# Kernel optimization log

Hardware: AMD Instinct MI355X
Metric: run time of the kernel (lower is better)

## Reference

```python
import jax, jax.numpy as jnp
import numpy as np
from jax import lax

B, CIN, H, W = 8, 3, 256, 256
CMID = 16          # conv out channels == config.in_channels
DM = 256           # d_model
P = 2              # patch size (hardcoded in Downsample)
DI = 512           # d_inner = expand * d_model
NH, HD, NS, KC = 8, 64, 128, 4   # heads, headdim, d_state, d_conv
CONVDIM = DI + 2 * NS            # 768
PROJ = 2 * DI + 2 * NS + NH      # 1288


def _sincos2d(dim, gs):
    # 2d sin-cos positional embedding, matches get_2d_sincos_pos_embed
    def emb1d(d, pos):
        omega = 1.0 / (10000.0 ** (jnp.arange(d // 2, dtype=jnp.float32) / (d / 2.0)))
        out = pos[:, None] * omega[None, :]
        return jnp.concatenate([jnp.sin(out), jnp.cos(out)], axis=1)
    g = jnp.arange(gs, dtype=jnp.float32)
    grid = jnp.stack(jnp.meshgrid(g, g), 0).reshape(2, -1)  # [2, gs*gs]
    return jnp.concatenate([emb1d(dim // 2, grid[0]), emb1d(dim // 2, grid[1])], 1)


def _mamba2(u, in_proj_w, conv1d_w, conv1d_b, dt_bias, A_log, D, norm_w, out_proj_w):
    b, l, _ = u.shape
    zxbcdt = jnp.einsum('bld,pd->blp', u, in_proj_w)              # [b,l,1288]
    z = zxbcdt[..., :DI]
    xBC = zxbcdt[..., DI:DI + CONVDIM]
    dt = zxbcdt[..., DI + CONVDIM:]                                # [b,l,NH]
    # causal depthwise conv1d over sequence, then SiLU
    xc = lax.conv_general_dilated(xBC.transpose(0, 2, 1), conv1d_w, (1,), [(KC - 1, 0)],
                                  feature_group_count=CONVDIM,
                                  dimension_numbers=('NCH', 'OIH', 'NCH'))
    xBC = jax.nn.silu(xc + conv1d_b[None, :, None]).transpose(0, 2, 1)
    xh = xBC[..., :DI].reshape(b, l, NH, HD)                       # [b,l,h,p]
    Bm = xBC[..., DI:DI + NS]                                      # [b,l,n]
    Cm = xBC[..., DI + NS:]                                        # [b,l,n]
    dt = jax.nn.softplus(dt + dt_bias)                             # [b,l,h]
    dA = jnp.exp(dt * (-jnp.exp(A_log)))                           # [b,l,h]
    dtx = dt[..., None] * xh                                       # [b,l,h,p]

    def step(s, inp):
        dtx_t, B_t, C_t, dA_t = inp
        s = s * dA_t[..., None, None] + dtx_t[..., None] * B_t[:, None, None, :]
        return s, jnp.einsum('bhpn,bn->bhp', s, C_t)

    s0 = jnp.zeros((b, NH, HD, NS), u.dtype)
    _, ys = lax.scan(step, s0, (dtx.transpose(1, 0, 2, 3), Bm.transpose(1, 0, 2),
                                Cm.transpose(1, 0, 2), dA.transpose(1, 0, 2)))
    y = ys.transpose(1, 0, 2, 3) + D[None, None, :, None] * xh     # [b,l,h,p]
    y = y.reshape(b, l, DI) * jax.nn.silu(z)                       # gated
    y = y * lax.rsqrt(jnp.mean(y * y, -1, keepdims=True) + 1e-5) * norm_w
    return jnp.einsum('bld,od->blo', y, out_proj_w)


def setup_inputs() -> dict:
    key = jax.random.key(0)
    ks = jax.random.split(key, 12)
    r = lambda i, s, sc: jax.random.normal(ks[i], s, jnp.float32) * sc
    return {
        'x': jax.random.normal(ks[0], (B, CIN, H, W), jnp.float32),
        'conv_w': r(1, (CMID, CIN, 3, 3), 0.1), 'conv_b': jnp.zeros((CMID,), jnp.float32),
        'bn_gamma': jnp.ones((CMID,), jnp.float32), 'bn_beta': jnp.zeros((CMID,), jnp.float32),
        'patch_w': r(2, (DM, CMID, P, P), 0.1), 'patch_b': jnp.zeros((DM,), jnp.float32),
        'in_proj_w': r(3, (PROJ, DM), 0.02),
        'conv1d_w': r(4, (CONVDIM, 1, KC), 0.1), 'conv1d_b': jnp.zeros((CONVDIM,), jnp.float32),
        'dt_bias': r(5, (NH,), 0.5),
        'A_log': jax.random.uniform(ks[6], (NH,), jnp.float32),
        'D': jnp.ones((NH,), jnp.float32),
        'norm_w': jnp.ones((DI,), jnp.float32),
        'out_proj_w': r(7, (DM, DI), 0.02),
        'final_w': r(8, (P * P * CMID, DM), 0.02), 'final_b': jnp.zeros((P * P * CMID,), jnp.float32),
    }


def reference(x, conv_w, conv_b, bn_gamma, bn_beta, patch_w, patch_b, in_proj_w,
              conv1d_w, conv1d_b, dt_bias, A_log, D, norm_w, out_proj_w, final_w, final_b):
    # Conv2d k=3 s=2 p=1 -> BatchNorm2d (training-mode batch stats) -> GELU
    h = lax.conv_general_dilated(x, conv_w, (2, 2), [(1, 1), (1, 1)],
                                 dimension_numbers=('NCHW', 'OIHW', 'NCHW')) + conv_b[None, :, None, None]
    mu = jnp.mean(h, (0, 2, 3), keepdims=True)
    var = jnp.var(h, (0, 2, 3), keepdims=True)
    h = (h - mu) * lax.rsqrt(var + 1e-5) * bn_gamma[None, :, None, None] + bn_beta[None, :, None, None]
    h = jax.nn.gelu(h, approximate=False)
    # PatchEmbed: conv k=p s=p, flatten to tokens, add frozen sincos pos embed
    t = lax.conv_general_dilated(h, patch_w, (P, P), 'VALID',
                                 dimension_numbers=('NCHW', 'OIHW', 'NCHW')) + patch_b[None, :, None, None]
    b, d, gh, gw = t.shape
    tok = t.reshape(b, d, gh * gw).transpose(0, 2, 1) + _sincos2d(DM, gh)[None]
    # MambaBlock: Mamba2(x) + x  (layers=1; repo loop discards all but last layer)
    y = _mamba2(tok, in_proj_w, conv1d_w, conv1d_b, dt_bias, A_log, D, norm_w, out_proj_w) + tok
    # FinalLayer: linear only (norm_final is unused in its forward)
    o = jnp.einsum('bld,od->blo', y, final_w) + final_b
    # unpatchify
    o = o.reshape(b, gh, gw, P, P, CMID)
    o = jnp.einsum('nhwpqc->nchpwq', o).reshape(b, CMID, gh * P, gw * P)
    return o
```

## Files before the change

kernel.cpp:

```cpp
#include <hip/hip_runtime.h>
#include <math.h>

#define B_  8
#define CIN 3
#define HIN 256
#define WIN 256
#define CMID 16
#define HMID 128
#define WMID 128
#define DM 256
#define L_ 4096
#define DI 512
#define NH 8
#define HD 64
#define NS 128
#define KC 4
#define CONVDIM 768
#define PROJ 1288
#define NPADIN 1408
#define MTOK (B_*L_)
#define QCH 128
#define NCH 32

typedef unsigned short bf16;
typedef __attribute__((ext_vector_type(8))) short bf16x8;
typedef __attribute__((ext_vector_type(4))) float f32x4;

__device__ inline float bf2f(bf16 u) { return __uint_as_float(((unsigned int)u) << 16); }
__device__ inline bf16 f2bf(float f) {
  unsigned int x = __float_as_uint(f);
  return (bf16)((x + 0x7fffu + ((x >> 16) & 1u)) >> 16);
}
__device__ inline unsigned int pack2bf(float a, float b) {
  return (unsigned int)f2bf(a) | ((unsigned int)f2bf(b) << 16);
}

__global__ void k_conv1(const float* __restrict__ x, const float* __restrict__ w,
                        const float* __restrict__ bias, float* __restrict__ out) {
  int idx = blockIdx.x*256 + threadIdx.x;
  if (idx >= B_*CMID*HMID*WMID) return;
  int xo = idx & 127, yo = (idx>>7)&127, co = (idx>>14)&15, b = idx>>18;
  float acc = bias[co];
  const float* xb = x + (size_t)b*CIN*HIN*WIN;
  const float* wc = w + co*CIN*9;
  #pragma unroll
  for (int ci=0; ci<CIN; ci++)
    #pragma unroll
    for (int ky=0; ky<3; ky++) {
      int yi = 2*yo - 1 + ky;
      if (yi < 0 || yi >= HIN) continue;
      #pragma unroll
      for (int kx=0; kx<3; kx++) {
        int xi = 2*xo - 1 + kx;
        if (xi < 0 || xi >= WIN) continue;
        acc += xb[(ci*HIN + yi)*WIN + xi] * wc[(ci*3+ky)*3+kx];
      }
    }
  out[idx] = acc;
}

__global__ __launch_bounds__(256) void k_bnstatsA(const float* __restrict__ h, float2* __restrict__ part) {
  int blk = blockIdx.x;
  const float4* base = (const float4*)(h + ((size_t)(blk>>2))*16384 + (blk&3)*4096);
  int tid = threadIdx.x;
  float s=0.f, s2=0.f;
  #pragma unroll
  for (int i=0;i<4;i++){
    float4 v = base[i*256 + tid];
    s += v.x+v.y+v.z+v.w;
    s2 += v.x*v.x + v.y*v.y + v.z*v.z + v.w*v.w;
  }
  #pragma unroll
  for (int off=1; off<64; off<<=1) { s += __shfl_xor(s, off); s2 += __shfl_xor(s2, off); }
  __shared__ float sb[2][4];
  if ((tid&63)==0){ sb[0][tid>>6]=s; sb[1][tid>>6]=s2; }
  __syncthreads();
  if (tid==0) part[blk] = make_float2(sb[0][0]+sb[0][1]+sb[0][2]+sb[0][3],
                                      sb[1][0]+sb[1][1]+sb[1][2]+sb[1][3]);
}

__global__ void k_bnstatsB(const float2* __restrict__ part, float* __restrict__ stats) {
  int lane = threadIdx.x;
  int c = lane >> 2, j0 = lane & 3;
  float s=0.f, s2=0.f;
  #pragma unroll
  for (int j=j0; j<32; j+=4){
    int b = j >> 2, chunk = j & 3;
    float2 p = part[(b*16+c)*4 + chunk];
    s += p.x; s2 += p.y;
  }
  s += __shfl_xor(s,1); s2 += __shfl_xor(s2,1);
  s += __shfl_xor(s,2); s2 += __shfl_xor(s2,2);
  if (j0==0){
    const float inv = 1.f/131072.f;
    float mean = s*inv;
    float var  = s2*inv - mean*mean;
    stats[c]      = mean;
    stats[16 + c] = rsqrtf(var + 1e-5f);
  }
}

__global__ __launch_bounds__(256) void k_patch(const float* __restrict__ h, const float* __restrict__ pw,
                       const float* __restrict__ pb, const float* __restrict__ stats,
                       const float* __restrict__ gamma, const float* __restrict__ beta,
                       bf16* __restrict__ tok) {
  int grp = blockIdx.x;
  int b = grp >> 9, g8 = grp & 511;
  int g0 = g8 << 3;
  int gy = g0 >> 6, gx0 = g0 & 63;
  __shared__ float sh[8][64];
  int tid = threadIdx.x;
  {
    int tk = tid >> 5, jj = (tid & 31)*2;
    int ci = jj >> 2, p = (jj >> 1) & 1;
    const float* src = &h[((size_t)(b*CMID+ci)*HMID + 2*gy+p)*WMID + 2*(gx0+tk)];
    float2 xv = *(const float2*)src;
    float mean = stats[ci], rstd = stats[16+ci];
    float sc = rstd*gamma[ci], be = beta[ci] - mean*sc;
    float v0 = xv.x*sc + be;
    float v1 = xv.y*sc + be;
    v0 = 0.5f*v0*(1.f + erff(v0*0.70710678118654752f));
    v1 = 0.5f*v1*(1.f + erff(v1*0.70710678118654752f));
    sh[tk][jj] = v0; sh[tk][jj+1] = v1;
  }
  __syncthreads();
  int d = tid;
  float wr[64];
  #pragma unroll
  for (int i4=0;i4<16;i4++) *(float4*)&wr[i4*4] = *(const float4*)&pw[d*64 + i4*4];
  float bias = pb[d];
  int i = d & 63;
  float omega = expf(-(float)i * (9.210340371976184f/64.f));
  #pragma unroll
  for (int tk=0;tk<8;tk++){
    float acc = bias;
    #pragma unroll
    for (int j=0;j<64;j++) acc = fmaf(sh[tk][j], wr[j], acc);
    float gv = (d < 128) ? (float)(gx0+tk) : (float)gy;
    float ph = gv * omega;
    float pos = (d & 64) ? __cosf(ph) : __sinf(ph);
    tok[((size_t)((b<<12) + g0 + tk))*DM + d] = f2bf(acc + pos);
  }
}

__global__ void k_cvtw(const float* __restrict__ src, bf16* __restrict__ dst,
                       int N, int kshift, int total) {
  int idx = blockIdx.x*256 + threadIdx.x;
  if (idx >= total) return;
  int n = idx >> kshift;
  dst[idx] = (n < N) ? f2bf(src[idx]) : (bf16)0;
}

template<int EPI>
__global__ __launch_bounds__(512) void k_mgemm(
    const bf16* __restrict__ A, const bf16* __restrict__ Bw, int K,
    bf16* __restrict__ o_z, bf16* __restrict__ o_x,
    bf16* __restrict__ o_y, const bf16* __restrict__ res,
    const float* __restrict__ dt_bias, const float* __restrict__ A_log,
    float* __restrict__ dtv, float* __restrict__ dAv,
    float* __restrict__ o_f, const float* __restrict__ fbias) {
  __shared__ __align__(16) char smem[49152];
  bf16* sA = (bf16*)smem;
  bf16* sB = (bf16*)(smem + 32768);
  bf16* sT = (bf16*)smem;
  int tid = threadIdx.x;
  int lane = tid & 63, wid = tid >> 6;
  int wr = wid >> 1, wc = wid & 1;
  int m0 = blockIdx.x*256, n0 = blockIdx.y*128;
  int nk = K >> 5;

  f32x4 acc[4][4];
  #pragma unroll
  for (int i=0;i<4;i++)
    #pragma unroll
    for (int j=0;j<4;j++)
      acc[i][j] = (f32x4){0.f,0.f,0.f,0.f};

  auto stage = [&](int buf, int ks){
    int kk = ks << 5;
    #pragma unroll
    for (int i=0;i<2;i++){
      int j = i*512 + tid;
      int row = j >> 2, cc = j & 3;
      int kg = cc ^ (row & 3);
      unsigned ldsoff = (unsigned)(buf*16384 + (i*512 + wid*64) * 16);
      __builtin_amdgcn_global_load_lds(
        (const __attribute__((address_space(1))) void*)(A + (size_t)(m0+row)*K + kk + kg*8),
        (__attribute__((address_space(3))) void*)((char*)sA + ldsoff), 16, 0, 0);
    }
    {
      int row = tid >> 2, cc = tid & 3;
      int kg = cc ^ (row & 3);
      unsigned ldsoff = (unsigned)(buf*8192 + (wid*64) * 16);
      __builtin_amdgcn_global_load_lds(
        (const __attribute__((address_space(1))) void*)(Bw + (size_t)(n0+row)*K + kk + kg*8),
        (__attribute__((address_space(3))) void*)((char*)sB + ldsoff), 16, 0, 0);
    }
  };

  int r = lane & 15, q = lane >> 4;
  int kgo = (q ^ (r & 3)) << 3;

  stage(0, 0);
  for (int ks=0; ks<nk; ++ks){
    int cur = ks & 1;
    __syncthreads();
    if (ks+1 < nk) stage(cur^1, ks+1);
    bf16x8 af[4], bfv[4];
    #pragma unroll
    for (int a=0;a<4;a++){
      int rown = wc*64 + a*16 + r;
      af[a] = *(const bf16x8*)&sB[cur*4096 + rown*32 + kgo];
    }
    #pragma unroll
    for (int bfr=0;bfr<4;bfr++){
      int rowm = wr*64 + bfr*16 + r;
      bfv[bfr] = *(const bf16x8*)&sA[cur*8192 + rowm*32 + kgo];
    }
    #pragma unroll
    for (int a=0;a<4;a++)
      #pragma unroll
      for (int bfr=0;bfr<4;bfr++)
        acc[a][bfr] = __builtin_amdgcn_mfma_f32_16x16x32_bf16(af[a], bfv[bfr], acc[a][bfr], 0, 0, 0);
  }

  if (EPI == 0 && n0 >= DI + CONVDIM) {
    #pragma unroll
    for (int a=0;a<4;a++){
      int n4 = n0 + wc*64 + a*16 + q*4;
      if (n4 >= PROJ) continue;
      #pragma unroll
      for (int bfr=0;bfr<4;bfr++){
        int m = m0 + wr*64 + bfr*16 + r;
        f32x4 v = acc[a][bfr];
        #pragma unroll
        for (int rr=0;rr<4;rr++){
          int hh = n4 + rr - (DI + CONVDIM);
          if (hh < NH){
            float xv = v[rr] + dt_bias[hh];
            float dt = (xv > 20.f) ? xv : log1pf(expf(xv));
            dtv[(size_t)m*NH + hh] = dt;
            dAv[(size_t)m*NH + hh] = expf(-expf(A_log[hh]) * dt);
          }
        }
      }
    }
    return;
  }

  #pragma unroll
  for (int h2=0; h2<2; ++h2){
    __syncthreads();
    if (wc == h2){
      #pragma unroll
      for (int a=0;a<4;a++){
        int nl = a*16 + q*4;
        #pragma unroll
        for (int bfr=0;bfr<4;bfr++){
          int ml = wr*64 + bfr*16 + r;
          f32x4 v = acc[a][bfr];
          *(uint2*)&sT[ml*72 + nl] = make_uint2(pack2bf(v[0],v[1]), pack2bf(v[2],v[3]));
        }
      }
    }
    __syncthreads();
    int ml = tid >> 1, ch = tid & 1;
    int m = m0 + ml;
    int ncol = n0 + h2*64 + ch*32;
    const bf16* src = &sT[ml*72 + ch*32];
    bf16* dst = (n0 < DI) ? (o_z + (size_t)m*DI + ncol)
                          : (o_x + (size_t)m*CONVDIM + (ncol - DI));
    #pragma unroll
    for (int i4=0;i4<4;i4++)
      *(uint4*)(dst + i4*8) = *(const uint4*)(src + i4*8);
  }
}

__global__ __launch_bounds__(512) void k_mgemm12(
    const bf16* __restrict__ A, const bf16* __restrict__ Bw,
    const bf16* __restrict__ res, const bf16* __restrict__ wfin,
    const float* __restrict__ fbias, float* __restrict__ o_f) {
  __shared__ __align__(16) char smem[49152];
  bf16* sA = (bf16*)smem;
  bf16* sB = (bf16*)(smem + 16384);
  bf16* sY = (bf16*)smem;
  int tid = threadIdx.x;
  int lane = tid & 63, wid = tid >> 6;
  int wr = wid >> 2, wc = wid & 3;
  int m0 = blockIdx.x*128;
  const int K = DI;
  int nk = K >> 5;

  f32x4 acc[4][4];
  #pragma unroll
  for (int i=0;i<4;i++)
    #pragma unroll
    for (int j=0;j<4;j++)
      acc[i][j] = (f32x4){0.f,0.f,0.f,0.f};

  auto stage = [&](int buf, int ks){
    int kk = ks << 5;
    {
      int row = tid >> 2, cc = tid & 3;
      int kg = cc ^ (row & 3);
      unsigned ldsoff = (unsigned)(buf*8192 + (wid*64) * 16);
      __builtin_amdgcn_global_load_lds(
        (const __attribute__((address_space(1))) void*)(A + (size_t)(m0+row)*K + kk + kg*8),
        (__attribute__((address_space(3))) void*)((char*)sA + ldsoff), 16, 0, 0);
    }
    #pragma unroll
    for (int i=0;i<2;i++){
      int j = i*512 + tid;
      int row = j >> 2, cc = j & 3;
      int kg = cc ^ (row & 3);
      unsigned ldsoff = (unsigned)(buf*16384 + (i*512 + wid*64) * 16);
      __builtin_amdgcn_global_load_lds(
        (const __attribute__((address_space(1))) void*)(Bw + (size_t)row*K + kk + kg*8),
        (__attribute__((address_space(3))) void*)((char*)sB + ldsoff), 16, 0, 0);
    }
  };

  int r = lane & 15, q = lane >> 4;
  int kgo = (q ^ (r & 3)) << 3;

  stage(0, 0);
  for (int ks=0; ks<nk; ++ks){
    int cur = ks & 1;
    __syncthreads();
    if (ks+1 < nk) stage(cur^1, ks+1);
    bf16x8 af[4], bfv[4];
    #pragma unroll
    for (int a=0;a<4;a++){
      int rown = wc*64 + a*16 + r;
      af[a] = *(const bf16x8*)&sB[cur*8192 + rown*32 + kgo];
    }
    #pragma unroll
    for (int mf=0;mf<4;mf++){
      int rowm = wr*64 + mf*16 + r;
      bfv[mf] = *(const bf16x8*)&sA[cur*4096 + rowm*32 + kgo];
    }
    #pragma unroll
    for (int a=0;a<4;a++)
      #pragma unroll
      for (int mf=0;mf<4;mf++)
        acc[a][mf] = __builtin_amdgcn_mfma_f32_16x16x32_bf16(af[a], bfv[mf], acc[a][mf], 0, 0, 0);
  }

  f32x4 acc2[4];
  #pragma unroll
  for (int i=0;i<4;i++) acc2[i] = (f32x4){0.f,0.f,0.f,0.f};
  int orow = wc*16 + r;

  #pragma unroll
  for (int j=0;j<4;j++){
    __syncthreads();
    if (wc == j){
      #pragma unroll
      for (int a=0;a<4;a++){
        int kl = a*16 + q*4;
        int chunk = kl >> 3, sub = (q & 1)*4;
        #pragma unroll
        for (int mf=0;mf<4;mf++){
          int ml = wr*64 + mf*16 + r;
          int m = m0 + ml;
          int n4 = wc*64 + kl;
          uint2 rv = *(const uint2*)(res + (size_t)m*DM + n4);
          f32x4 v = acc[a][mf];
          float y0 = v[0] + bf2f((bf16)(rv.x & 0xffffu));
          float y1 = v[1] + bf2f((bf16)(rv.x >> 16));
          float y2 = v[2] + bf2f((bf16)(rv.y & 0xffffu));
          float y3 = v[3] + bf2f((bf16)(rv.y >> 16));
          *(uint2*)&sY[ml*64 + ((chunk ^ (ml&7))<<3) + sub] =
              make_uint2(pack2bf(y0,y1), pack2bf(y2,y3));
        }
      }
    }
    __syncthreads();
    #pragma unroll
    for (int kstep=0;kstep<2;kstep++){
      bf16x8 af2 = *(const bf16x8*)(wfin + (size_t)orow*DM + j*64 + kstep*32 + q*8);
      #pragma unroll
      for (int mf=0;mf<4;mf++){
        int ml = wr*64 + mf*16 + r;
        int cg = kstep*4 + q;
        bf16x8 bv = *(const bf16x8*)&sY[ml*64 + ((cg ^ (ml&7))<<3)];
        acc2[mf] = __builtin_amdgcn_mfma_f32_16x16x32_bf16(af2, bv, acc2[mf], 0, 0, 0);
      }
    }
  }

  #pragma unroll
  for (int mf=0;mf<4;mf++){
    int m = m0 + wr*64 + mf*16 + r;
    int b = m >> 12, g = m & 4095;
    int gy = g >> 6, gx = g & 63;
    f32x4 v = acc2[mf];
    #pragma unroll
    for (int rr=0;rr<4;rr++){
      int o = wc*16 + q*4 + rr;
      float vv = v[rr] + fbias[o];
      int p = o >> 5, qq = (o>>4)&1, cc2 = o & 15;
      o_f[(((size_t)(b*CMID+cc2))*HMID + 2*gy+p)*WMID + (2*gx+qq)] = vv;
    }
  }
}

__global__ __launch_bounds__(256) void k_conv1d(const bf16* __restrict__ xpre, const float* __restrict__ cw,
                         const float* __restrict__ cb, bf16* __restrict__ xbc) {
  int idx = blockIdx.x*256 + threadIdx.x;
  int gch = idx % 96;
  int tb  = idx / 96;
  int ch0 = gch*8;
  int bl0 = tb*8;
  int l0 = bl0 & (L_-1);
  float wv[32];
  #pragma unroll
  for (int i=0;i<8;i++) *(float4*)&wv[i*4] = *(const float4*)&cw[ch0*KC + i*4];
  float bs[8];
  *(float4*)&bs[0] = *(const float4*)&cb[ch0];
  *(float4*)&bs[4] = *(const float4*)&cb[ch0+4];
  uint4 rows[11];
  #pragma unroll
  for (int j=0;j<11;j++){
    int lk = l0 - 3 + j;
    if (lk < 0) rows[j] = make_uint4(0u,0u,0u,0u);
    else rows[j] = *(const uint4*)(xpre + ((size_t)bl0 - 3 + j)*CONVDIM + ch0);
  }
  #pragma unroll
  for (int t=0;t<8;t++){
    float acc[8];
    #pragma unroll
    for (int i=0;i<8;i++) acc[i] = bs[i];
    #pragma unroll
    for (int k=0;k<KC;k++){
      uint4 u = rows[t+k];
      unsigned uu[4]={u.x,u.y,u.z,u.w};
      #pragma unroll
      for (int c2=0;c2<4;c2++){
        float lo = __uint_as_float(uu[c2]<<16);
        float hi = __uint_as_float(uu[c2]&0xffff0000u);
        acc[c2*2]   = fmaf(wv[(c2*2)*4 + k],   lo, acc[c2*2]);
        acc[c2*2+1] = fmaf(wv[(c2*2+1)*4 + k], hi, acc[c2*2+1]);
      }
    }
    unsigned ou[4];
    #pragma unroll
    for (int c2=0;c2<4;c2++){
      float v0 = acc[c2*2], v1 = acc[c2*2+1];
      v0 = v0 / (1.f + __expf(-v0));
      v1 = v1 / (1.f + __expf(-v1));
      ou[c2] = pack2bf(v0, v1);
    }
    *(uint4*)(xbc + (size_t)(bl0+t)*CONVDIM + ch0) = make_uint4(ou[0],ou[1],ou[2],ou[3]);
  }
}

__global__ __launch_bounds__(512) void k_ssd1(const bf16* __restrict__ xbc,
    const float* __restrict__ dtv, const float* __restrict__ A_log,
    bf16* __restrict__ ys, bf16* __restrict__ Sst) {
  int blk = blockIdx.x;
  int c = blk & (NCH-1), h = (blk>>5)&7, b = blk>>8;
  int tid = threadIdx.x;
  int lane = tid & 63, wid = tid >> 6;
  int r = lane & 15, q = lane >> 4;
  size_t rowbase = (size_t)b*L_ + (size_t)c*QCH;
  float eA = __expf(A_log[h]);

  __shared__ __align__(16) char smem[81920];
  bf16* sB  = (bf16*)smem;
  bf16* sC  = (bf16*)(smem + 32768);
  bf16* sDX = (bf16*)(smem + 65536);
  float* fDT = (float*)(smem + 65536);
  float* fL  = fDT + 128;
  float* fWS = fL + 128;
  float* fWT = fWS + 128;

  #pragma unroll
  for (int i=0;i<8;i++){
    int id = i*512 + tid;
    int row = id >> 5, cg = id & 31;
    uint4 u = *(const uint4*)(xbc + (rowbase+row)*CONVDIM + DI + cg*8);
    if (cg < 16) *(uint4*)&sB[row*128 + ((cg ^ (row&15))<<3)] = u;
    else { int cg2 = cg-16; *(uint4*)&sC[row*128 + ((cg2 ^ (row&15))<<3)] = u; }
  }
  if (tid < 128) fDT[tid] = dtv[(rowbase+tid)*NH + h];
  __syncthreads();

  float inc = 0.f;
  if (tid < 128){
    inc = fDT[tid];
    #pragma unroll
    for (int off=1; off<64; off<<=1){
      float u = __shfl_up(inc, off);
      if (lane >= off) inc += u;
    }
    if (lane==63) fWT[wid] = inc;
  }
  __syncthreads();
  if (tid < 128){
    if (wid==1) inc += fWT[0];
    fL[tid] = inc;
  }

  int wr = wid >> 1, wc = wid & 1;
  f32x4 accG[2][4];
  #pragma unroll
  for (int i=0;i<2;i++)
    #pragma unroll
    for (int j=0;j<4;j++) accG[i][j] = (f32x4){0.f,0.f,0.f,0.f};
  #pragma unroll
  for (int ks=0; ks<4; ks++){
    bf16x8 af[2], bfv[4];
    #pragma unroll
    for (int mf=0;mf<2;mf++){
      int s = wr*32 + mf*16 + r;
      af[mf] = *(const bf16x8*)&sB[s*128 + (((ks*4+q) ^ (s&15))<<3)];
    }
    #pragma unroll
    for (int nf=0;nf<4;nf++){
      int t = wc*64 + nf*16 + r;
      bfv[nf] = *(const bf16x8*)&sC[t*128 + (((ks*4+q) ^ (t&15))<<3)];
    }
    #pragma unroll
    for (int mf=0;mf<2;mf++)
      #pragma unroll
      for (int nf=0;nf<4;nf++)
        accG[mf][nf] = __builtin_amdgcn_mfma_f32_16x16x32_bf16(af[mf], bfv[nf], accG[mf][nf], 0, 0, 0);
  }
  __syncthreads();

  bf16* sW = sC;
  #pragma unroll
  for (int mf=0;mf<2;mf++){
    int sb4 = wr*32 + mf*16 + q*4;
    int cb4 = sb4 >> 3, se4 = sb4 & 7;
    #pragma unroll
    for (int nf=0;nf<4;nf++){
      int t = wc*64 + nf*16 + r;
      float Lt = fL[t];
      float w[4];
      #pragma unroll
      for (int rr=0;rr<4;rr++){
        int s = sb4 + rr;
        float v = 0.f;
        if (s <= t) v = accG[mf][nf][rr] * fDT[s] * __expf(-eA*(Lt - fL[s]));
        w[rr] = v;
      }
      *(uint2*)&sW[t*128 + ((cb4 ^ (t&15))<<3) + se4] =
          make_uint2(pack2bf(w[0],w[1]), pack2bf(w[2],w[3]));
    }
  }
  if (tid < 128) fWS[tid] = fDT[tid]*__expf(-eA*(fL[127]-fL[tid]));
  __syncthreads();

  int nT = tid >> 2, sg = tid & 3;
  unsigned short vals[32];
  #pragma unroll
  for (int i8=0;i8<4;i8++){
    #pragma unroll
    for (int j=0;j<8;j++){
      int s = sg*32 + i8*8 + j;
      float bv = bf2f(sB[s*128 + (((nT>>3) ^ (s&15))<<3) + (nT&7)]);
      vals[i8*8+j] = f2bf(bv * fWS[s]);
    }
  }
  __syncthreads();

  #pragma unroll
  for (int i8=0;i8<4;i8++){
    int s8 = sg*4 + i8;
    *(uint4*)&sB[nT*128 + ((s8 ^ (nT&15))<<3)] = *(const uint4*)&vals[i8*8];
  }
  {
    int s0 = (tid >> 3)*2;
    int p0 = (tid & 7)*8;
    const bf16* x0 = xbc + (rowbase+s0)*CONVDIM + h*HD + p0;
    uint4 u0 = *(const uint4*)x0;
    uint4 u1 = *(const uint4*)(x0 + CONVDIM);
    unsigned a0[4]={u0.x,u0.y,u0.z,u0.w}, a1[4]={u1.x,u1.y,u1.z,u1.w};
    int cb2 = s0 >> 3, se = s0 & 7;
    #pragma unroll
    for (int jp=0;jp<4;jp++){
      unsigned w0=a0[jp], w1=a1[jp];
      unsigned lo = (w0 & 0xffffu) | (w1 << 16);
      unsigned hi = (w0 >> 16) | (w1 & 0xffff0000u);
      int pA = p0 + jp*2, pB = pA+1;
      *(unsigned*)&sDX[pA*128 + ((cb2 ^ (pA&15))<<3) + se] = lo;
      *(unsigned*)&sDX[pB*128 + ((cb2 ^ (pB&15))<<3) + se] = hi;
    }
  }
  __syncthreads();

  {
    int wrp = wid >> 2, wct = wid & 3;
    f32x4 acc2[2][2];
    #pragma unroll
    for (int i=0;i<2;i++){ acc2[i][0]=(f32x4){0.f,0.f,0.f,0.f}; acc2[i][1]=(f32x4){0.f,0.f,0.f,0.f}; }
    #pragma unroll
    for (int ks=0; ks<4; ks++){
      bf16x8 af[2], bfv[2];
      #pragma unroll
      for (int mf=0;mf<2;mf++){
        int p = wrp*32 + mf*16 + r;
        af[mf] = *(const bf16x8*)&sDX[p*128 + (((ks*4+q) ^ (p&15))<<3)];
      }
      #pragma unroll
      for (int nf=0;nf<2;nf++){
        int t = wct*32 + nf*16 + r;
        bfv[nf] = *(const bf16x8*)&sW[t*128 + (((ks*4+q) ^ (t&15))<<3)];
      }
      #pragma unroll
      for (int mf=0;mf<2;mf++)
        #pragma unroll
        for (int nf=0;nf<2;nf++)
          acc2[mf][nf] = __builtin_amdgcn_mfma_f32_16x16x32_bf16(af[mf], bfv[nf], acc2[mf][nf], 0, 0, 0);
    }
    #pragma unroll
    for (int mf=0;mf<2;mf++){
      int pb = wrp*32 + mf*16 + q*4;
      #pragma unroll
      for (int nf=0;nf<2;nf++){
        int t = wct*32 + nf*16 + r;
        f32x4 v = acc2[mf][nf];
        *(uint2*)(ys + (rowbase+t)*DI + h*HD + pb) =
            make_uint2(pack2bf(v[0],v[1]), pack2bf(v[2],v[3]));
      }
    }
  }
  {
    int wrn = wid >> 1, wcp = wid & 1;
    f32x4 acc3[2][2];
    #pragma unroll
    for (int i=0;i<2;i++){ acc3[i][0]=(f32x4){0.f,0.f,0.f,0.f}; acc3[i][1]=(f32x4){0.f,0.f,0.f,0.f}; }
    #pragma unroll
    for (int ks=0; ks<4; ks++){
      bf16x8 af[2], bfv[2];
      #pragma unroll
      for (int mf=0;mf<2;mf++){
        int n = wrn*32 + mf*16 + r;
        af[mf] = *(const bf16x8*)&sB[n*128 + (((ks*4+q) ^ (n&15))<<3)];
      }
      #pragma unroll
      for (int nf=0;nf<2;nf++){
        int p = wcp*32 + nf*16 + r;
        bfv[nf] = *(const bf16x8*)&sDX[p*128 + (((ks*4+q) ^ (p&15))<<3)];
      }
      #pragma unroll
      for (int mf=0;mf<2;mf++)
        #pragma unroll
        for (int nf=0;nf<2;nf++)
          acc3[mf][nf] = __builtin_amdgcn_mfma_f32_16x16x32_bf16(af[mf], bfv[nf], acc3[mf][nf], 0, 0, 0);
    }
    size_t sb = (((size_t)(b*NH+h))*NCH + c)*8192;
    #pragma unroll
    for (int mf=0;mf<2;mf++){
      int nb = wrn*32 + mf*16 + q*4;
      #pragma unroll
      for (int nf=0;nf<2;nf++){
        int p = wcp*32 + nf*16 + r;
        f32x4 v = acc3[mf][nf];
        *(uint2*)(Sst + sb + (size_t)p*128 + nb) =
            make_uint2(pack2bf(v[0],v[1]), pack2bf(v[2],v[3]));
      }
    }
  }
}

template<int NCHT, int QCHT>
__global__ __launch_bounds__(256) void k_scan2(bf16* __restrict__ Sst, const float* __restrict__ dAv) {
  constexpr int SEG = QCHT/16;
  int blk = blockIdx.x;
  int bh = blk>>2, q = blk&3;
  int b = bh>>3, h = bh&7;
  int tid = threadIdx.x;
  __shared__ float sP[NCHT];
  {
    int c = tid / SEG, seg = tid & (SEG-1);
    float prod = 1.f;
    size_t base = ((size_t)b*L_ + c*QCHT + seg*16)*NH + h;
    #pragma unroll
    for (int k=0;k<16;k++) prod *= dAv[base + (size_t)k*NH];
    #pragma unroll
    for (int off=1; off<SEG; off<<=1) prod *= __shfl_xor(prod, off);
    if (seg==0) sP[c] = prod;
  }
  __syncthreads();
  int e0 = q*2048 + tid*8;
  float acc[8];
  #pragma unroll
  for (int j=0;j<8;j++) acc[j]=0.f;
  size_t sbase = (size_t)bh*NCHT*8192 + e0;
  for (int c=0;c<NCHT;c++){
    bf16* ptr = Sst + sbase + (size_t)c*8192;
    uint4 u = *(const uint4*)ptr;
    unsigned int uu[4] = {u.x,u.y,u.z,u.w};
    float tv[8];
    #pragma unroll
    for (int k=0;k<4;k++){
      tv[2*k]   = __uint_as_float(uu[k]<<16);
      tv[2*k+1] = __uint_as_float(uu[k]&0xffff0000u);
    }
    uint4 o;
    o.x = pack2bf(acc[0],acc[1]); o.y = pack2bf(acc[2],acc[3]);
    o.z = pack2bf(acc[4],acc[5]); o.w = pack2bf(acc[6],acc[7]);
    asm volatile("s_waitcnt vmcnt(0)" ::: "memory");
    *(uint4*)ptr = o;
    float P = sP[c];
    #pragma unroll
    for (int j=0;j<8;j++) acc[j] = tv[j] + P*acc[j];
  }
}

__global__ __launch_bounds__(256) void k_ssd3(const bf16* __restrict__ xbc,
    const float* __restrict__ dtv, const float* __restrict__ A_log,
    const bf16* __restrict__ Sst, bf16* __restrict__ ys) {
  int blk = blockIdx.x;
  int c = blk & (NCH-1), h = (blk>>5)&7, b = blk>>8;
  int tid = threadIdx.x;
  int lane = tid & 63, wid = tid >> 6;
  int r = lane & 15, q = lane >> 4;
  size_t rowbase = (size_t)b*L_ + (size_t)c*QCH;
  float eA = __expf(A_log[h]);

  __shared__ __align__(16) bf16 sC[128*128];
  __shared__ float sDT[128];
  __shared__ float sAt[128];
  __shared__ float sWT[2];

  #pragma unroll
  for (int i=0;i<8;i++){
    int id = i*256 + tid;
    int row = id >> 4, cg = id & 15;
    uint4 u = *(const uint4*)(xbc + (rowbase+row)*CONVDIM + DI + NS + cg*8);
    *(uint4*)&sC[row*128 + ((cg ^ (row&15))<<3)] = u;
  }
  if (tid < 128) sDT[tid] = dtv[(rowbase+tid)*NH + h];
  __syncthreads();
  float inc = 0.f;
  if (tid < 128){
    inc = sDT[tid];
    #pragma unroll
    for (int off=1; off<64; off<<=1){
      float u = __shfl_up(inc, off);
      if (lane >= off) inc += u;
    }
    if (lane==63) sWT[wid] = inc;
  }
  __syncthreads();
  if (tid < 128){
    if (wid==1) inc += sWT[0];
    sAt[tid] = __expf(-eA*inc);
  }
  __syncthreads();

  int wrp = wid >> 1, wct = wid & 1;
  size_t sb = (((size_t)(b*NH+h))*NCH + c)*8192;
  f32x4 accP[2][4];
  #pragma unroll
  for (int i=0;i<2;i++)
    #pragma unroll
    for (int j=0;j<4;j++) accP[i][j] = (f32x4){0.f,0.f,0.f,0.f};
  #pragma unroll
  for (int ks=0; ks<4; ks++){
    bf16x8 af[2], bfv[4];
    #pragma unroll
    for (int mf=0;mf<2;mf++){
      int p = wrp*32 + mf*16 + r;
      af[mf] = *(const bf16x8*)(Sst + sb + (size_t)p*128 + ks*32 + q*8);
    }
    #pragma unroll
    for (int nf=0;nf<4;nf++){
      int t = wct*64 + nf*16 + r;
      bfv[nf] = *(const bf16x8*)&sC[t*128 + (((ks*4+q) ^ (t&15))<<3)];
    }
    #pragma unroll
    for (int mf=0;mf<2;mf++)
      #pragma unroll
      for (int nf=0;nf<4;nf++)
        accP[mf][nf] = __builtin_amdgcn_mfma_f32_16x16x32_bf16(af[mf], bfv[nf], accP[mf][nf], 0, 0, 0);
  }
  #pragma unroll
  for (int mf=0;mf<2;mf++){
    int pb = wrp*32 + mf*16 + q*4;
    #pragma unroll
    for (int nf=0;nf<4;nf++){
      int t = wct*64 + nf*16 + r;
      float at = sAt[t];
      bf16* yp = ys + (rowbase+t)*DI + h*HD + pb;
      uint2 old = *(uint2*)yp;
      float o0 = bf2f((bf16)(old.x & 0xffffu))  + at*accP[mf][nf][0];
      float o1 = bf2f((bf16)(old.x >> 16))      + at*accP[mf][nf][1];
      float o2 = bf2f((bf16)(old.y & 0xffffu))  + at*accP[mf][nf][2];
      float o3 = bf2f((bf16)(old.y >> 16))      + at*accP[mf][nf][3];
      *(uint2*)yp = make_uint2(pack2bf(o0,o1), pack2bf(o2,o3));
    }
  }
}

__global__ __launch_bounds__(256) void k_combine(bf16* __restrict__ ys, const bf16* __restrict__ xbc,
                         const bf16* __restrict__ z, const float* __restrict__ Dp,
                         const float* __restrict__ nw) {
  int bl = blockIdx.x;
  int tid = threadIdx.x;
  bf16* yrow = ys + (size_t)bl*DI;
  const bf16* xrow = xbc + (size_t)bl*CONVDIM;
  const bf16* zrow = z + (size_t)bl*DI;
  float v[2]; float ss = 0.f;
  #pragma unroll
  for (int i=0;i<2;i++) {
    int d = tid + i*256;
    float xh = bf2f(xrow[d]);
    float y = bf2f(yrow[d]) + Dp[d>>6]*xh;
    float zv = bf2f(zrow[d]);
    y *= zv / (1.f + expf(-zv));
    v[i] = y; ss += y*y;
  }
  #pragma unroll
  for (int off=1; off<64; off<<=1) ss += __shfl_xor(ss, off);
  __shared__ float sb[4];
  if ((tid&63)==0) sb[tid>>6]=ss;
  __syncthreads();
  float total = sb[0]+sb[1]+sb[2]+sb[3];
  float scale = rsqrtf(total * (1.f/512.f) + 1e-5f);
  #pragma unroll
  for (int i=0;i<2;i++) {
    int d = tid + i*256;
    yrow[d] = f2bf(v[i]*scale*nw[d]);
  }
}

extern "C" void kernel_launch(void* const* d_in, const int* in_sizes, int n_in,
                              void* d_out, int out_size, void* d_ws, size_t ws_size,
                              hipStream_t stream) {
  const float* x         = (const float*)d_in[0];
  const float* conv_w    = (const float*)d_in[1];
  const float* conv_b    = (const float*)d_in[2];
  const float* bn_gamma  = (const float*)d_in[3];
  const float* bn_beta   = (const float*)d_in[4];
  const float* patch_w   = (const float*)d_in[5];
  const float* patch_b   = (const float*)d_in[6];
  const float* in_proj_w = (const float*)d_in[7];
  const float* conv1d_w  = (const float*)d_in[8];
  const float* conv1d_b  = (const float*)d_in[9];
  const float* dt_bias   = (const float*)d_in[10];
  const float* A_log     = (const float*)d_in[11];
  const float* Dp        = (const float*)d_in[12];
  const float* norm_w    = (const float*)d_in[13];
  const float* out_proj_w= (const float*)d_in[14];
  const float* final_w   = (const float*)d_in[15];
  const float* final_b   = (const float*)d_in[16];
  float* out = (float*)d_out;

  char* Wb = (char*)d_ws;
  float* h_buf = (float*)(Wb + 0);
  bf16*  winb  = (bf16*)(Wb + 0);
  bf16*  woutb = (bf16*)(Wb + 0);
  bf16*  wfinb = (bf16*)(Wb + 262144);
  bf16*  xpost = (bf16*)(Wb + 0);
  float2* part = (float2*)(Wb + 50331648);
  bf16*  tok   = (bf16*)(Wb + 50331648);
  bf16*  zbuf  = (bf16*)(Wb + 67108864);
  bf16*  xpre  = (bf16*)(Wb + 100663296);
  bf16*  ysb   = (bf16*)(Wb + 100663296);
  bf16*  Sst   = (bf16*)(Wb + 134217728);
  float* dtv   = (float*)(Wb + 134217728 + 33554432);
  float* dAv   = dtv + 262144;
  float* stats = dAv + 262144;
  const size_t NEED = 134217728ull + 33554432 + 2097152 + 256;
  if (ws_size < NEED) {
    hipMemsetAsync(d_out, 0, (size_t)out_size*sizeof(float), stream);
    return;
  }

  k_conv1<<<dim3((B_*CMID*HMID*WMID)/256), dim3(256), 0, stream>>>(x, conv_w, conv_b, h_buf);
  k_bnstatsA<<<dim3(512), dim3(256), 0, stream>>>(h_buf, part);
  k_bnstatsB<<<dim3(1), dim3(64), 0, stream>>>(part, stats);
  k_patch<<<dim3(MTOK/8), dim3(256), 0, stream>>>(h_buf, patch_w, patch_b, stats, bn_gamma, bn_beta, tok);
  k_cvtw<<<dim3((NPADIN*DM)/256), dim3(256), 0, stream>>>(in_proj_w, winb, PROJ, 8, NPADIN*DM);
  k_mgemm<0><<<dim3(MTOK/256, NPADIN/128), dim3(512), 0, stream>>>(tok, winb, DM,
      zbuf, xpre, nullptr, nullptr, dt_bias, A_log, dtv, dAv, nullptr, nullptr);
  k_conv1d<<<dim3((MTOK/8*96)/256), dim3(256), 0, stream>>>(xpre, conv1d_w, conv1d_b, xpost);
  k_ssd1<<<dim3(B_*NH*NCH), dim3(512), 0, stream>>>(xpost, dtv, A_log, ysb, Sst);
  k_scan2<NCH,QCH><<<dim3(B_*NH*4), dim3(256), 0, stream>>>(Sst, dAv);
  k_ssd3<<<dim3(B_*NH*NCH), dim3(256), 0, stream>>>(xpost, dtv, A_log, Sst, ysb);
  k_combine<<<dim3(MTOK), dim3(256), 0, stream>>>(ysb, xpost, zbuf, Dp, norm_w);
  k_cvtw<<<dim3((DM*DI)/256), dim3(256), 0, stream>>>(out_proj_w, woutb, DM, 9, DM*DI);
  k_cvtw<<<dim3((128*DM)/256), dim3(256), 0, stream>>>(final_w, wfinb, 64, 8, 128*DM);
  k_mgemm12<<<dim3(MTOK/128), dim3(512), 0, stream>>>(ysb, woutb, tok, wfinb, final_b, out);
}
```

Measured before the change: 324.6 us.

## Fuse causal depthwise conv1d and SiLU into the in_proj GEMM epilogue

```diff
diff --git a/kernel.cpp b/kernel.cpp
--- a/kernel.cpp
+++ b/kernel.cpp
@@ -151,18 +151,18 @@
   dst[idx] = (n < N) ? f2bf(src[idx]) : (bf16)0;
 }
 
-template<int EPI>
-__global__ __launch_bounds__(512) void k_mgemm(
-    const bf16* __restrict__ A, const bf16* __restrict__ Bw, int K,
+__global__ __launch_bounds__(512) void k_mgemm0(
+    const bf16* __restrict__ A, const bf16* __restrict__ Bw,
     bf16* __restrict__ o_z, bf16* __restrict__ o_x,
-    bf16* __restrict__ o_y, const bf16* __restrict__ res,
+    const float* __restrict__ cw, const float* __restrict__ cb,
     const float* __restrict__ dt_bias, const float* __restrict__ A_log,
-    float* __restrict__ dtv, float* __restrict__ dAv,
-    float* __restrict__ o_f, const float* __restrict__ fbias) {
+    float* __restrict__ dtv, float* __restrict__ dAv) {
+  const int K = DM;
   __shared__ __align__(16) char smem[49152];
   bf16* sA = (bf16*)smem;
   bf16* sB = (bf16*)(smem + 32768);
   bf16* sT = (bf16*)smem;
+  bf16* sH = (bf16*)(smem + 36864);
   int tid = threadIdx.x;
   int lane = tid & 63, wid = tid >> 6;
   int wr = wid >> 1, wc = wid & 1;
@@ -224,7 +224,7 @@
         acc[a][bfr] = __builtin_amdgcn_mfma_f32_16x16x32_bf16(af[a], bfv[bfr], acc[a][bfr], 0, 0, 0);
   }
 
-  if (EPI == 0 && n0 >= DI + CONVDIM) {
+  if (n0 >= DI + CONVDIM) {
     #pragma unroll
     for (int a=0;a<4;a++){
       int n4 = n0 + wc*64 + a*16 + q*4;
@@ -248,6 +248,33 @@
     return;
   }
 
+  bool isx = (n0 >= DI);
+  bool bstart = ((m0 & 4095) == 0);
+
+  if (isx && tid < 384) {
+    int j = tid >> 7, col = tid & 127;
+    float d = 0.f;
+    if (!bstart) {
+      const bf16* ar = A + (size_t)(m0 - 3 + j)*K;
+      const bf16* br = Bw + (size_t)(n0 + col)*K;
+      for (int k2=0;k2<K/8;k2++){
+        ushort4 a0 = *(const ushort4*)(ar + k2*8);
+        ushort4 a1 = *(const ushort4*)(ar + k2*8 + 4);
+        ushort4 b0 = *(const ushort4*)(br + k2*8);
+        ushort4 b1 = *(const ushort4*)(br + k2*8 + 4);
+        d = fmaf(bf2f(a0.x), bf2f(b0.x), d);
+        d = fmaf(bf2f(a0.y), bf2f(b0.y), d);
+        d = fmaf(bf2f(a0.z), bf2f(b0.z), d);
+        d = fmaf(bf2f(a0.w), bf2f(b0.w), d);
+        d = fmaf(bf2f(a1.x), bf2f(b1.x), d);
+        d = fmaf(bf2f(a1.y), bf2f(b1.y), d);
+        d = fmaf(bf2f(a1.z), bf2f(b1.z), d);
+        d = fmaf(bf2f(a1.w), bf2f(b1.w), d);
+      }
+    }
+    sH[j*128 + col] = f2bf(d);
+  }
+
   #pragma unroll
   for (int h2=0; h2<2; ++h2){
     __syncthreads();
@@ -266,13 +293,51 @@
     __syncthreads();
     int ml = tid >> 1, ch = tid & 1;
     int m = m0 + ml;
-    int ncol = n0 + h2*64 + ch*32;
-    const bf16* src = &sT[ml*72 + ch*32];
-    bf16* dst = (n0 < DI) ? (o_z + (size_t)m*DI + ncol)
-                          : (o_x + (size_t)m*CONVDIM + (ncol - DI));
-    #pragma unroll
-    for (int i4=0;i4<4;i4++)
-      *(uint4*)(dst + i4*8) = *(const uint4*)(src + i4*8);
+    if (!isx) {
+      int ncol = n0 + h2*64 + ch*32;
+      const bf16* src = &sT[ml*72 + ch*32];
+      bf16* dst = o_z + (size_t)m*DI + ncol;
+      #pragma unroll
+      for (int i4=0;i4<4;i4++)
+        *(uint4*)(dst + i4*8) = *(const uint4*)(src + i4*8);
+    } else {
+      int colb = (n0 - DI) + h2*64 + ch*32;
+      int hoff = h2*64 + ch*32;
+      #pragma unroll
+      for (int g=0; g<4; ++g){
+        int c0 = g*8;
+        uint4 rv[4];
+        #pragma unroll
+        for (int k=0;k<4;k++){
+          int mm = ml - 3 + k;
+          if (mm >= 0) rv[k] = *(const uint4*)&sT[mm*72 + ch*32 + c0];
+          else if (bstart) rv[k] = make_uint4(0u,0u,0u,0u);
+          else rv[k] = *(const uint4*)&sH[(3+mm)*128 + hoff + c0];
+        }
+        unsigned ou[4];
+        #pragma unroll
+        for (int cp=0;cp<4;cp++){
+          int cA = colb + c0 + 2*cp, cB = cA + 1;
+          float4 w0 = *(const float4*)&cw[cA*4];
+          float4 w1 = *(const float4*)&cw[cB*4];
+          float a0 = cb[cA], a1 = cb[cB];
+          float wk0[4] = {w0.x,w0.y,w0.z,w0.w};
+          float wk1[4] = {w1.x,w1.y,w1.z,w1.w};
+          #pragma unroll
+          for (int k=0;k<4;k++){
+            unsigned uw = ((const unsigned*)&rv[k])[cp];
+            float lo = __uint_as_float(uw<<16);
+            float hi = __uint_as_float(uw & 0xffff0000u);
+            a0 = fmaf(wk0[k], lo, a0);
+            a1 = fmaf(wk1[k], hi, a1);
+          }
+          a0 = a0/(1.f+__expf(-a0));
+          a1 = a1/(1.f+__expf(-a1));
+          ou[cp] = pack2bf(a0,a1);
+        }
+        *(uint4*)(o_x + (size_t)m*CONVDIM + colb + c0) = make_uint4(ou[0],ou[1],ou[2],ou[3]);
+      }
+    }
   }
 }
 
@@ -402,56 +467,6 @@
       int p = o >> 5, qq = (o>>4)&1, cc2 = o & 15;
       o_f[(((size_t)(b*CMID+cc2))*HMID + 2*gy+p)*WMID + (2*gx+qq)] = vv;
     }
-  }
-}
-
-__global__ __launch_bounds__(256) void k_conv1d(const bf16* __restrict__ xpre, const float* __restrict__ cw,
-                         const float* __restrict__ cb, bf16* __restrict__ xbc) {
-  int idx = blockIdx.x*256 + threadIdx.x;
-  int gch = idx % 96;
-  int tb  = idx / 96;
-  int ch0 = gch*8;
-  int bl0 = tb*8;
-  int l0 = bl0 & (L_-1);
-  float wv[32];
-  #pragma unroll
-  for (int i=0;i<8;i++) *(float4*)&wv[i*4] = *(const float4*)&cw[ch0*KC + i*4];
-  float bs[8];
-  *(float4*)&bs[0] = *(const float4*)&cb[ch0];
-  *(float4*)&bs[4] = *(const float4*)&cb[ch0+4];
-  uint4 rows[11];
-  #pragma unroll
-  for (int j=0;j<11;j++){
-    int lk = l0 - 3 + j;
-    if (lk < 0) rows[j] = make_uint4(0u,0u,0u,0u);
-    else rows[j] = *(const uint4*)(xpre + ((size_t)bl0 - 3 + j)*CONVDIM + ch0);
-  }
-  #pragma unroll
-  for (int t=0;t<8;t++){
-    float acc[8];
-    #pragma unroll
-    for (int i=0;i<8;i++) acc[i] = bs[i];
-    #pragma unroll
-    for (int k=0;k<KC;k++){
-      uint4 u = rows[t+k];
-      unsigned uu[4]={u.x,u.y,u.z,u.w};
-      #pragma unroll
-      for (int c2=0;c2<4;c2++){
-        float lo = __uint_as_float(uu[c2]<<16);
-        float hi = __uint_as_float(uu[c2]&0xffff0000u);
-        acc[c2*2]   = fmaf(wv[(c2*2)*4 + k],   lo, acc[c2*2]);
-        acc[c2*2+1] = fmaf(wv[(c2*2+1)*4 + k], hi, acc[c2*2+1]);
-      }
-    }
-    unsigned ou[4];
-    #pragma unroll
-    for (int c2=0;c2<4;c2++){
-      float v0 = acc[c2*2], v1 = acc[c2*2+1];
-      v0 = v0 / (1.f + __expf(-v0));
-      v1 = v1 / (1.f + __expf(-v1));
-      ou[c2] = pack2bf(v0, v1);
-    }
-    *(uint4*)(xbc + (size_t)(bl0+t)*CONVDIM + ch0) = make_uint4(ou[0],ou[1],ou[2],ou[3]);
   }
 }
 
@@ -853,16 +868,15 @@
 
   char* Wb = (char*)d_ws;
   float* h_buf = (float*)(Wb + 0);
-  bf16*  winb  = (bf16*)(Wb + 0);
   bf16*  woutb = (bf16*)(Wb + 0);
   bf16*  wfinb = (bf16*)(Wb + 262144);
   bf16*  xpost = (bf16*)(Wb + 0);
   float2* part = (float2*)(Wb + 50331648);
   bf16*  tok   = (bf16*)(Wb + 50331648);
   bf16*  zbuf  = (bf16*)(Wb + 67108864);
-  bf16*  xpre  = (bf16*)(Wb + 100663296);
   bf16*  ysb   = (bf16*)(Wb + 100663296);
   bf16*  Sst   = (bf16*)(Wb + 134217728);
+  bf16*  winb  = (bf16*)(Wb + 134217728);
   float* dtv   = (float*)(Wb + 134217728 + 33554432);
   float* dAv   = dtv + 262144;
   float* stats = dAv + 262144;
@@ -877,9 +891,8 @@
   k_bnstatsB<<<dim3(1), dim3(64), 0, stream>>>(part, stats);
   k_patch<<<dim3(MTOK/8), dim3(256), 0, stream>>>(h_buf, patch_w, patch_b, stats, bn_gamma, bn_beta, tok);
   k_cvtw<<<dim3((NPADIN*DM)/256), dim3(256), 0, stream>>>(in_proj_w, winb, PROJ, 8, NPADIN*DM);
-  k_mgemm<0><<<dim3(MTOK/256, NPADIN/128), dim3(512), 0, stream>>>(tok, winb, DM,
-      zbuf, xpre, nullptr, nullptr, dt_bias, A_log, dtv, dAv, nullptr, nullptr);
-  k_conv1d<<<dim3((MTOK/8*96)/256), dim3(256), 0, stream>>>(xpre, conv1d_w, conv1d_b, xpost);
+  k_mgemm0<<<dim3(MTOK/256, NPADIN/128), dim3(512), 0, stream>>>(tok, winb,
+      zbuf, xpost, conv1d_w, conv1d_b, dt_bias, A_log, dtv, dAv);
   k_ssd1<<<dim3(B_*NH*NCH), dim3(512), 0, stream>>>(xpost, dtv, A_log, ysb, Sst);
   k_scan2<NCH,QCH><<<dim3(B_*NH*4), dim3(256), 0, stream>>>(Sst, dAv);
   k_ssd3<<<dim3(B_*NH*NCH), dim3(256), 0, stream>>>(xpost, dtv, A_log, Sst, ysb);
```

Result: slower. 353.8 us (+9.0%).
